# Optimization experiments

Measured on AMD Instinct MI355X. Metric: run time of the kernel, lower is better.

## Reference

```python
import jax, jax.numpy as jnp
import numpy as np

N = 20000   # nodes
E = 320000  # edges
T = 12      # sequence_length
H = 64      # hidden_dim
CIN = 16    # input_dim_per_step
L = 3       # num_st_layers
BN_EPS = 1e-5


def setup_inputs() -> dict:
    key = jax.random.key(0)
    ks = jax.random.split(key, 30)
    s = 0.05
    rn = lambda k, shp: jax.random.normal(k, shp, jnp.float32) * s
    inp = {
        "x": jax.random.normal(ks[0], (N, T * CIN), jnp.float32),
        "edge_index": jax.random.randint(ks[1], (2, E), 0, N, jnp.int32),
        # embedding
        "We": rn(ks[2], (CIN, H)), "be": rn(ks[3], (H,)),
        # stacked per-layer params for the 3 ST layers
        "gcn_W": rn(ks[4], (L, H, H)), "gcn_b": rn(ks[5], (L, H)),
        "conv_w": rn(ks[6], (L, H, H, 3)), "conv_b": rn(ks[7], (L, H)),
        "bn_g": jnp.ones((L, H), jnp.float32), "bn_b": rn(ks[8], (L, H)),
        "bn_m": rn(ks[9], (L, H)),
        "bn_v": jax.random.uniform(ks[10], (L, H), jnp.float32, 0.5, 1.5),
        # temporal attention MLP (H -> H//2 -> 1)
        "ta_w1": rn(ks[11], (H, H // 2)), "ta_b1": rn(ks[12], (H // 2,)),
        "ta_w2": rn(ks[13], (H // 2, 1)), "ta_b2": rn(ks[14], (1,)),
        # feature attention MLP (T -> T//2 -> 1)
        "fa_w1": rn(ks[15], (T, T // 2)), "fa_b1": rn(ks[16], (T // 2,)),
        "fa_w2": rn(ks[17], (T // 2, 1)), "fa_b2": rn(ks[18], (1,)),
        # output MLP (H -> H//2 -> 1)
        "ow1": rn(ks[19], (H, H // 2)), "ob1": rn(ks[20], (H // 2,)),
        "ow2": rn(ks[21], (H // 2, 1)), "ob2": rn(ks[22], (1,)),
    }
    return inp


def reference(x, edge_index, We, be, gcn_W, gcn_b, conv_w, conv_b,
              bn_g, bn_b, bn_m, bn_v, ta_w1, ta_b1, ta_w2, ta_b2,
              fa_w1, fa_b1, fa_w2, fa_b2, ow1, ob1, ow2, ob2):
    n = x.shape[0]
    # --- GCN normalization with self-loops (PyG gcn_norm) ---
    loops = jnp.arange(n, dtype=edge_index.dtype)
    src = jnp.concatenate([edge_index[0], loops])
    dst = jnp.concatenate([edge_index[1], loops])
    deg = jax.ops.segment_sum(jnp.ones_like(src, jnp.float32), dst, num_segments=n)
    dinv = 1.0 / jnp.sqrt(deg)  # deg >= 1 thanks to self-loops
    coef = dinv[src] * dinv[dst]  # [E+N]

    # --- per-timestep embedding (vectorized over t) ---
    xr = x.reshape(n, T, CIN)
    emb = jax.nn.relu(jnp.einsum('ntc,ch->nth', xr, We) + be)  # [N,T,H]
    x_st = emb.reshape(n, T * H)

    # --- ST layers (replicating original row-major .view layout mixing) ---
    for i in range(L):
        xi = x_st.reshape(n, H, T)  # [N,C,T]
        # GCNConv per timestep, batched over t: linear then normalized aggregate
        h = jnp.einsum('nct,cd->ndt', xi, gcn_W[i])          # [N,H,T]
        msg = coef[:, None, None] * h[src]                   # [E+N,H,T]
        agg = jax.ops.segment_sum(msg, dst, num_segments=n) + gcn_b[i][None, :, None]
        # temporal conv (kernel 3, pad 1) over T
        tmp = jax.lax.conv_general_dilated(
            agg, conv_w[i], (1,), [(1, 1)],
            dimension_numbers=('NCH', 'OIH', 'NCH')) + conv_b[i][None, :, None]
        # BatchNorm1d (eval mode: running stats)
        normed = (tmp - bn_m[i][None, :, None]) / jnp.sqrt(bn_v[i][None, :, None] + BN_EPS)
        normed = normed * bn_g[i][None, :, None] + bn_b[i][None, :, None]
        # residual is Identity (in_channels == out_channels)
        x_st = jax.nn.relu(normed + xi).reshape(n, H * T)

    # --- dual attention pooling ---
    xa = x_st.reshape(n, T, H)
    tw = (jnp.einsum('ntm,mk->ntk', jax.nn.relu(jnp.einsum('nth,hm->ntm', xa, ta_w1) + ta_b1), ta_w2) + ta_b2)[..., 0]
    tw = jax.nn.softmax(tw, axis=1)                          # [N,T]
    xt = (xa * tw[..., None]).transpose(0, 2, 1)             # [N,H,T]
    fw = (jnp.einsum('nhm,mk->nhk', jax.nn.relu(jnp.einsum('nht,tm->nhm', xt, fa_w1) + fa_b1), fa_w2) + fa_b2)[..., 0]
    fw = jax.nn.softmax(fw, axis=1)                          # [N,H]
    x_final = jnp.sum(xt * fw[..., None], axis=2)            # [N,H]

    # --- output MLP (dropout is identity in eval) ---
    out = jax.nn.relu(x_final @ ow1 + ob1) @ ow2 + ob2       # [N,1]
    return out
```

## Files before the change

### kernel.cpp

```cpp
#include <hip/hip_runtime.h>
#include <cstddef>
#include <cstdint>

#define T_ 12
#define H_ 64
#define CIN_ 16
#define F_ 768
#define BN_EPS 1e-5f
#define ECAP 80
#define RPITCH 88
#define SLOTS 64

typedef float v2f __attribute__((ext_vector_type(2)));
typedef short s8v __attribute__((ext_vector_type(8)));
typedef float f4v __attribute__((ext_vector_type(4)));

__device__ __forceinline__ unsigned short f2bf(float f) {
    unsigned u = __float_as_uint(f);
    unsigned r = (u + 0x7FFFu + ((u >> 16) & 1u)) >> 16;
    return (unsigned short)r;
}
__device__ __forceinline__ float bf2f(unsigned short h) {
    return __uint_as_float(((unsigned)h) << 16);
}
__device__ __forceinline__ v2f bf2x2(unsigned u) {
    v2f r;
    r.x = __uint_as_float(u << 16);
    r.y = __uint_as_float(u & 0xFFFF0000u);
    return r;
}
__device__ __forceinline__ v2f pkfma(v2f a, v2f b, v2f c) {
    return __builtin_elementwise_fma(a, b, c);
}


__global__ void k_init(int* __restrict__ cursor, int n) {
    int i = blockIdx.x * 256 + threadIdx.x;
    if (i < n) cursor[i] = 0;
}


__global__ __launch_bounds__(256) void k_fused(
        const float* __restrict__ gcn_W, const float* __restrict__ gcn_b,
        const float* __restrict__ conv_w,
        unsigned short* __restrict__ wkA, float* __restrict__ bkp,
        const int* __restrict__ srcv, const int* __restrict__ dstv,
        int* __restrict__ cursor, int* __restrict__ csr_src, int e,
        const float* __restrict__ x, const float* __restrict__ We,
        const float* __restrict__ be, unsigned short* __restrict__ xbf, int nT,
        int nbE) {
    __shared__ float smem[5312];
    int b = blockIdx.x;
    int tid = threadIdx.x;

    if (b < 36) {
        int l = b / 12, k = (b / 4) % 3, cq = b & 3;
        const float* Wg = gcn_W + (size_t)l * 4096;
        const float* cw = conv_w + (size_t)l * 12288;
        float* scwT = smem;
        float* sWg  = smem + 4224;
        float* sgb  = smem + 5248;
        for (int i = tid; i < 4096; i += 256)
            scwT[(i & 63) * 66 + (i >> 6)] = cw[(size_t)i * 3 + k];
        for (int i = tid; i < 1024; i += 256)
            sWg[i] = Wg[cq * 16 * 64 + i];
        if (tid < 64) sgb[tid] = gcn_b[(size_t)l * 64 + tid];
        __syncthreads();
#pragma unroll
        for (int j = 0; j < 4; j++) {
            int idx = j * 256 + tid;
            int cc = idx >> 6;
            int o  = idx & 63;
            float acc = 0.f;
            for (int d = 0; d < 64; d++)
                acc += sWg[cc * 64 + d] * scwT[d * 66 + o];
            int cful = cq * 16 + cc;
            int kidx = k * 64 + cful;
            int ks = kidx >> 5, r = kidx & 31;
            int ln = (r >> 3) * 16 + (o & 15);
            int jj = r & 7;
            wkA[((((size_t)l * 24) + (o >> 4) * 6 + ks) * 64 + ln) * 8 + jj] =
                f2bf(acc);
        }
        if (cq == 0 && tid < 64) {
            int o = tid;
            float acc = 0.f;
            for (int d = 0; d < 64; d++)
                acc += sgb[d] * scwT[d * 66 + o];
            bkp[((size_t)l * 3 + k) * 64 + o] = acc;
        }
        return;
    }
    if (b < 36 + nbE) {
        int i = (b - 36) * 256 + tid;
        if (i < e) {
            int d = dstv[i], s = srcv[i];
            int pos = atomicAdd(&cursor[d], 1);
            if (pos < SLOTS) csr_src[d * SLOTS + pos] = s;
        }
        return;
    }
    float* sW = smem;
    float* sb = smem + 1024;
    for (int i = tid; i < CIN_ * H_; i += 256) sW[i] = We[i];
    if (tid < H_) sb[tid] = be[tid];
    __syncthreads();
    int h4  = tid & 15;
    int ntl = tid >> 4;
    int nt  = (b - 36 - nbE) * 16 + ntl;
    if (nt >= nT) return;
    const float4* xp = (const float4*)(x + (size_t)nt * CIN_);
    float4 xv4[4];
    xv4[0] = xp[0]; xv4[1] = xp[1]; xv4[2] = xp[2]; xv4[3] = xp[3];
    const float* xs = (const float*)xv4;
    float acc[4];
#pragma unroll
    for (int j = 0; j < 4; j++) acc[j] = sb[h4 * 4 + j];
#pragma unroll
    for (int c = 0; c < CIN_; c++) {
        float4 w = *(const float4*)&sW[c * H_ + h4 * 4];
        float xc = xs[c];
        acc[0] += xc * w.x; acc[1] += xc * w.y;
        acc[2] += xc * w.z; acc[3] += xc * w.w;
    }
    ushort4 h;
    h.x = f2bf(fmaxf(acc[0], 0.f)); h.y = f2bf(fmaxf(acc[1], 0.f));
    h.z = f2bf(fmaxf(acc[2], 0.f)); h.w = f2bf(fmaxf(acc[3], 0.f));
    *(ushort4*)&xbf[(size_t)nt * H_ + h4 * 4] = h;
}


__global__ __launch_bounds__(256) void k_post(
        const int* __restrict__ cursor, const int* __restrict__ csr_src,
        float* __restrict__ csr_coef, float* __restrict__ dinv, int n) {
    int i = blockIdx.x * 256 + threadIdx.x;
    int node = i >> 6, slot = i & 63;
    if (node >= n) return;
    int deg = cursor[node];
    float dn = rsqrtf((float)(deg + 1));
    if (slot == 0) dinv[node] = dn;
    if (slot < min(deg, SLOTS)) {
        int s = csr_src[node * SLOTS + slot];
        csr_coef[node * SLOTS + slot] = rsqrtf((float)(cursor[s] + 1)) * dn;
    }
}


#define BPK(aL, aH, c2, u) { \
    aL = pkfma(bf2x2((u).x), c2, aL); \
    aH = pkfma(bf2x2((u).y), c2, aH); }

#define LAYER_GATHER_CONV()                                                    \
    int tid = threadIdx.x;                                                     \
    int n0 = blockIdx.x * 8;                                                   \
    int wave = tid >> 6, lane = tid & 63;                                      \
    int wbase = wave * (ECAP * 2);                                             \
    for (int i = tid; i < 8 * 2 * RPITCH; i += 256) {                          \
        int s = i / (2 * RPITCH);                                              \
        int r = i - s * (2 * RPITCH);                                          \
        int row = (r < RPITCH) ? 0 : 13;                                       \
        int c = (r < RPITCH) ? r : r - RPITCH;                                 \
        sxb[s * 14 * RPITCH + row * RPITCH + c] = 0;                           \
    }                                                                          \
    int begs[2], cnts[2], stgs[2], epos[2];                                    \
    {                                                                          \
        int pos = 0;                                                           \
        for (int si = 0; si < 2; si++) {                                       \
            int nn = n0 + wave * 2 + si; if (nn >= n) nn = n - 1;              \
            int beg = nn * SLOTS;                                              \
            int cnt = min(degv[nn], SLOTS);                                    \
            int stg = min(cnt, ECAP - pos);                                    \
            for (int i = lane; i < stg; i += 64) {                             \
                se[wbase + (pos + i) * 2]     = csr_src[beg + i] * F_;         \
                se[wbase + (pos + i) * 2 + 1] = __float_as_int(csr_coef[beg + i]); \
            }                                                                  \
            begs[si] = beg; cnts[si] = cnt; stgs[si] = stg; epos[si] = pos;    \
            pos += stg;                                                        \
        }                                                                      \
    }                                                                          \
    {                                                                          \
        int i0 = 3 * lane;                                                     \
        for (int si = 0; si < 2; si++) {                                       \
            int s = wave * 2 + si;                                             \
            int nn = n0 + s; if (nn >= n) nn = n - 1;                          \
            float dn = dinv[nn];                                               \
            float cs = dn * dn;                                                \
            v2f cs2 = {cs, cs};                                                \
            const uint2* xp = (const uint2*)(xin + (size_t)nn * F_);           \
            uint2 u0 = xp[i0], u1 = xp[i0 + 1], u2 = xp[i0 + 2];               \
            v2f a0 = bf2x2(u0.x) * cs2, a1 = bf2x2(u0.y) * cs2;                \
            v2f a2 = bf2x2(u1.x) * cs2, a3 = bf2x2(u1.y) * cs2;                \
            v2f a4 = bf2x2(u2.x) * cs2, a5 = bf2x2(u2.y) * cs2;                \
            int cnt = stgs[si];                                                \
            int base = wbase + epos[si] * 2;                                   \
            int e = 0;                                                         \
            for (; e + 3 < cnt; e += 4) {                                      \
                int2 p0 = *(const int2*)&se[base + e * 2];                     \
                int2 p1 = *(const int2*)&se[base + e * 2 + 2];                 \
                int2 p2 = *(const int2*)&se[base + e * 2 + 4];                 \
                int2 p3 = *(const int2*)&se[base + e * 2 + 6];                 \
                const uint2* pA = (const uint2*)(xin + p0.x);                  \
                const uint2* pB = (const uint2*)(xin + p1.x);                  \
                const uint2* pC = (const uint2*)(xin + p2.x);                  \
                const uint2* pD = (const uint2*)(xin + p3.x);                  \
                uint2 uA0 = pA[i0], uA1 = pA[i0 + 1], uA2 = pA[i0 + 2];        \
                uint2 uB0 = pB[i0], uB1 = pB[i0 + 1], uB2 = pB[i0 + 2];        \
                uint2 uC0 = pC[i0], uC1 = pC[i0 + 1], uC2 = pC[i0 + 2];        \
                uint2 uD0 = pD[i0], uD1 = pD[i0 + 1], uD2 = pD[i0 + 2];        \
                float cA = __int_as_float(p0.y), cB = __int_as_float(p1.y);    \
                float cC = __int_as_float(p2.y), cD = __int_as_float(p3.y);    \
                v2f cA2 = {cA, cA}, cB2 = {cB, cB};                            \
                v2f cC2 = {cC, cC}, cD2 = {cD, cD};                            \
                BPK(a0, a1, cA2, uA0) BPK(a2, a3, cA2, uA1) BPK(a4, a5, cA2, uA2) \
                BPK(a0, a1, cB2, uB0) BPK(a2, a3, cB2, uB1) BPK(a4, a5, cB2, uB2) \
                BPK(a0, a1, cC2, uC0) BPK(a2, a3, cC2, uC1) BPK(a4, a5, cC2, uC2) \
                BPK(a0, a1, cD2, uD0) BPK(a2, a3, cD2, uD1) BPK(a4, a5, cD2, uD2) \
            }                                                                  \
            for (; e < cnt; e++) {                                             \
                int2 p0 = *(const int2*)&se[base + e * 2];                     \
                const uint2* pA = (const uint2*)(xin + p0.x);                  \
                uint2 uA0 = pA[i0], uA1 = pA[i0 + 1], uA2 = pA[i0 + 2];        \
                float cA = __int_as_float(p0.y);                               \
                v2f cA2 = {cA, cA};                                            \
                BPK(a0, a1, cA2, uA0) BPK(a2, a3, cA2, uA1) BPK(a4, a5, cA2, uA2) \
            }                                                                  \
            for (int g = begs[si] + stgs[si]; g < begs[si] + cnts[si]; g++) {  \
                int srcO = csr_src[g] * F_;                                    \
                float cf = csr_coef[g];                                        \
                const uint2* pA = (const uint2*)(xin + srcO);                  \
                uint2 uA0 = pA[i0], uA1 = pA[i0 + 1], uA2 = pA[i0 + 2];        \
                v2f cf2 = {cf, cf};                                            \
                BPK(a0, a1, cf2, uA0) BPK(a2, a3, cf2, uA1) BPK(a4, a5, cf2, uA2) \
            }                                                                  \
            unsigned short* wp = &sxb[s * 14 * RPITCH + RPITCH + lane];        \
            float vals[12] = {a0.x, a0.y, a1.x, a1.y, a2.x, a2.y,              \
                              a3.x, a3.y, a4.x, a4.y, a5.x, a5.y};             \
            for (int t = 0; t < 12; t++) wp[t * RPITCH] = f2bf(vals[t]);       \
        }                                                                      \
    }                                                                          \
    __syncthreads();                                                           \
    int mt = wave;                                                             \
    int q = lane >> 4;                                                         \
    int l15 = lane & 15;                                                       \
    s8v afr[6];                                                                \
    const s8v* Ap = (const s8v*)wkA;                                           \
    for (int ks = 0; ks < 6; ks++) afr[ks] = Ap[(mt * 6 + ks) * 64 + lane];    \
    int obase = mt * 16 + q * 4;                                               \
    float scl[4], shf[4], ball[4], bk0a[4], bk2a[4];                           \
    for (int r = 0; r < 4; r++) {                                              \
        int o = obase + r;                                                     \
        float sc = bng[o] * rsqrtf(bnv[o] + BN_EPS);                           \
        scl[r] = sc;                                                           \
        shf[r] = bnb[o] - bnm[o] * sc;                                         \
        float b0 = bkp[o], b1 = bkp[64 + o], b2 = bkp[128 + o];                \
        ball[r] = cb[o] + b0 + b1 + b2;                                        \
        bk0a[r] = b0; bk2a[r] = b2;                                            \
    }                                                                          \
    f4v accv[6];                                                               \
    for (int nt = 0; nt < 6; nt++) {                                           \
        int nidx = nt * 16 + l15;                                              \
        int s = nidx / 12, t = nidx - 12 * s;                                  \
        const s8v* bp = (const s8v*)&sxb[s * 14 * RPITCH + t * RPITCH + q * 8];\
        f4v acc = {0.f, 0.f, 0.f, 0.f};                                        \
        acc = __builtin_amdgcn_mfma_f32_16x16x32_bf16(afr[0], bp[0],  acc, 0, 0, 0); \
        acc = __builtin_amdgcn_mfma_f32_16x16x32_bf16(afr[1], bp[4],  acc, 0, 0, 0); \
        acc = __builtin_amdgcn_mfma_f32_16x16x32_bf16(afr[2], bp[11], acc, 0, 0, 0); \
        acc = __builtin_amdgcn_mfma_f32_16x16x32_bf16(afr[3], bp[15], acc, 0, 0, 0); \
        acc = __builtin_amdgcn_mfma_f32_16x16x32_bf16(afr[4], bp[22], acc, 0, 0, 0); \
        acc = __builtin_amdgcn_mfma_f32_16x16x32_bf16(afr[5], bp[26], acc, 0, 0, 0); \
        accv[nt] = acc;                                                        \
    }                                                                          \
    __syncthreads();                                                           \
    for (int nt = 0; nt < 6; nt++) {                                           \
        int nidx = nt * 16 + l15;                                              \
        int s = nidx / 12, t = nidx - 12 * s;                                  \
        unsigned short* dp = &sxb[s * F_ + t];                                 \
        for (int r = 0; r < 4; r++) {                                          \
            float bias = ball[r];                                              \
            if (t == 0)  bias -= bk0a[r];                                      \
            if (t == 11) bias -= bk2a[r];                                      \
            float v = (accv[nt][r] + bias) * scl[r] + shf[r];                  \
            dp[(obase + r) * 12] = f2bf(v);                                    \
        }                                                                      \
    }                                                                          \
    __syncthreads();


__global__ __launch_bounds__(256, 7) void k_layer(
        const unsigned short* __restrict__ xin,
        unsigned short* __restrict__ xout,
        const int* __restrict__ degv, const int* __restrict__ csr_src,
        const float* __restrict__ csr_coef, const float* __restrict__ dinv,
        const unsigned short* __restrict__ wkA,
        const float* __restrict__ bkp, const float* __restrict__ cb,
        const float* __restrict__ bng, const float* __restrict__ bnb,
        const float* __restrict__ bnm, const float* __restrict__ bnv,
        int n) {
    __shared__ __align__(16) unsigned short sxb[8 * 14 * RPITCH];
    __shared__ int se[4 * ECAP * 2];
    LAYER_GATHER_CONV()

#pragma unroll
    for (int cidx = 0; cidx < 3; cidx++) {
        int c = cidx * 256 + tid;
        int s = c / 96, off = c - s * 96;
        int nn = n0 + s;
        if (nn >= n) continue;
        uint4 dv = *(const uint4*)&sxb[s * F_ + off * 8];
        uint4 rv = ((const uint4*)(xin + (size_t)nn * F_))[off];
        uint4 ov;
        unsigned* dvp = (unsigned*)&dv;
        unsigned* rvp = (unsigned*)&rv;
        unsigned* ovp = (unsigned*)&ov;
#pragma unroll
        for (int w = 0; w < 4; w++) {
            v2f d2 = bf2x2(dvp[w]);
            v2f r2 = bf2x2(rvp[w]);
            float lo = fmaxf(d2.x + r2.x, 0.f);
            float hi = fmaxf(d2.y + r2.y, 0.f);
            ovp[w] = (unsigned)f2bf(lo) | ((unsigned)f2bf(hi) << 16);
        }
        *(uint4*)(xout + (size_t)nn * F_ + off * 8) = ov;
    }
}


__global__ __launch_bounds__(256, 6) void k_layer_attn(
        const unsigned short* __restrict__ xin,
        const int* __restrict__ degv, const int* __restrict__ csr_src,
        const float* __restrict__ csr_coef, const float* __restrict__ dinv,
        const unsigned short* __restrict__ wkA,
        const float* __restrict__ bkp, const float* __restrict__ cb,
        const float* __restrict__ bng, const float* __restrict__ bnb,
        const float* __restrict__ bnm, const float* __restrict__ bnv,
        const float* __restrict__ taw1, const float* __restrict__ tab1,
        const float* __restrict__ taw2, const float* __restrict__ tab2,
        const float* __restrict__ faw1, const float* __restrict__ fab1,
        const float* __restrict__ faw2, const float* __restrict__ fab2,
        const float* __restrict__ ow1, const float* __restrict__ ob1,
        const float* __restrict__ ow2, const float* __restrict__ ob2,
        float* __restrict__ out, int n) {
    __shared__ __align__(16) unsigned short sxb[8 * 14 * RPITCH];
    __shared__ int se[4 * ECAP * 2];
    LAYER_GATHER_CONV()

#pragma unroll
    for (int cidx = 0; cidx < 3; cidx++) {
        int c = cidx * 256 + tid;
        int s = c / 96, off = c - s * 96;
        int nn = n0 + s; if (nn >= n) nn = n - 1;
        uint4 dv = *(const uint4*)&sxb[s * F_ + off * 8];
        uint4 rv = ((const uint4*)(xin + (size_t)nn * F_))[off];
        unsigned* dvp = (unsigned*)&dv;
        unsigned* rvp = (unsigned*)&rv;
#pragma unroll
        for (int w = 0; w < 4; w++) {
            v2f d2 = bf2x2(dvp[w]);
            v2f r2 = bf2x2(rvp[w]);
            float lo = fmaxf(d2.x + r2.x, 0.f);
            float hi = fmaxf(d2.y + r2.y, 0.f);
            dvp[w] = (unsigned)f2bf(lo) | ((unsigned)f2bf(hi) << 16);
        }
        *(uint4*)&sxb[s * F_ + off * 8] = dv;
    }
    __syncthreads();

    float* s_tw = (float*)se;
    float* s_xf = (float*)se + 96;

    {
        int s2 = tid >> 5, m = tid & 31;
        float bm = tab1[m];
        v2f aa0 = {bm, bm}, aa1 = aa0, aa2 = aa0;
        v2f aa3 = aa0, aa4 = aa0, aa5 = aa0;
        const unsigned short* xr = &sxb[s2 * F_];
        float tb2 = tab2[0];
        for (int hh = 0; hh < 64; hh++) {
            const uint2* xp2 = (const uint2*)&xr[hh * 12];
            uint2 w0 = xp2[0], w1 = xp2[1], w2 = xp2[2];
            float wv = taw1[hh * 32 + m];
            v2f wv2 = {wv, wv};
            aa0 = pkfma(bf2x2(w0.x), wv2, aa0);
            aa1 = pkfma(bf2x2(w0.y), wv2, aa1);
            aa2 = pkfma(bf2x2(w1.x), wv2, aa2);
            aa3 = pkfma(bf2x2(w1.y), wv2, aa3);
            aa4 = pkfma(bf2x2(w2.x), wv2, aa4);
            aa5 = pkfma(bf2x2(w2.y), wv2, aa5);
        }
        float w2v = taw2[m];
        float av[12] = {aa0.x, aa0.y, aa1.x, aa1.y, aa2.x, aa2.y,
                        aa3.x, aa3.y, aa4.x, aa4.y, aa5.x, aa5.y};
#pragma unroll
        for (int t = 0; t < 12; t++) {
            float p = fmaxf(av[t], 0.f) * w2v;
            p += __shfl_xor(p, 1); p += __shfl_xor(p, 2);
            p += __shfl_xor(p, 4); p += __shfl_xor(p, 8);
            p += __shfl_xor(p, 16);
            if (m == 0) s_tw[s2 * 12 + t] = p + tb2;
        }
    }
    __syncthreads();

    {
        float fb2 = fab2[0];
        for (int qi = 0; qi < 2; qi++) {
            int ss = wave * 2 + qi;
            float tw[12];
#pragma unroll
            for (int t = 0; t < 12; t++) tw[t] = s_tw[ss * 12 + t];
            float mx = tw[0];
#pragma unroll
            for (int t = 1; t < 12; t++) mx = fmaxf(mx, tw[t]);
            float sum = 0.f;
#pragma unroll
            for (int t = 0; t < 12; t++) { tw[t] = __expf(tw[t] - mx); sum += tw[t]; }
            float inv = 1.f / sum;
            const uint2* xp2 = (const uint2*)&sxb[ss * F_ + lane * 12];
            uint2 w0 = xp2[0], w1 = xp2[1], w2 = xp2[2];
            v2f x0 = bf2x2(w0.x), x1 = bf2x2(w0.y), x2 = bf2x2(w1.x);
            v2f x3 = bf2x2(w1.y), x4 = bf2x2(w2.x), x5 = bf2x2(w2.y);
            float xv[12] = {x0.x, x0.y, x1.x, x1.y, x2.x, x2.y,
                            x3.x, x3.y, x4.x, x4.y, x5.x, x5.y};
            float xt[12];
#pragma unroll
            for (int t = 0; t < 12; t++) xt[t] = xv[t] * tw[t] * inv;
            float lf = fb2;
#pragma unroll
            for (int mm = 0; mm < 6; mm++) {
                float v = fab1[mm];
#pragma unroll
                for (int t = 0; t < 12; t++) v += xt[t] * faw1[t * 6 + mm];
                lf += fmaxf(v, 0.f) * faw2[mm];
            }
            float m2v = lf;
#pragma unroll
            for (int off = 32; off >= 1; off >>= 1)
                m2v = fmaxf(m2v, __shfl_xor(m2v, off));
            float ev = __expf(lf - m2v);
            float sev = ev;
#pragma unroll
            for (int off = 32; off >= 1; off >>= 1) sev += __shfl_xor(sev, off);
            float fwv = ev / sev;
            float xs = 0.f;
#pragma unroll
            for (int t = 0; t < 12; t++) xs += xt[t];
            s_xf[ss * 65 + lane] = fwv * xs;
        }
    }
    __syncthreads();

    {
        int s2 = tid >> 5, m = tid & 31;
        float v = ob1[m];
        const float* xfp = &s_xf[s2 * 65];
        for (int hh = 0; hh < 64; hh++) v += xfp[hh] * ow1[hh * 32 + m];
        float p = fmaxf(v, 0.f) * ow2[m];
        p += __shfl_xor(p, 1); p += __shfl_xor(p, 2);
        p += __shfl_xor(p, 4); p += __shfl_xor(p, 8);
        p += __shfl_xor(p, 16);
        if (m == 0 && n0 + s2 < n) out[n0 + s2] = p + ob2[0];
    }
}


extern "C" void kernel_launch(void* const* d_in, const int* in_sizes, int n_in,
                              void* d_out, int out_size, void* d_ws, size_t ws_size,
                              hipStream_t stream) {
    const float* x      = (const float*)d_in[0];
    const int*   ei     = (const int*)d_in[1];
    const float* We     = (const float*)d_in[2];
    const float* be     = (const float*)d_in[3];
    const float* gcn_W  = (const float*)d_in[4];
    const float* gcn_b  = (const float*)d_in[5];
    const float* conv_w = (const float*)d_in[6];
    const float* conv_b = (const float*)d_in[7];
    const float* bn_g   = (const float*)d_in[8];
    const float* bn_b   = (const float*)d_in[9];
    const float* bn_m   = (const float*)d_in[10];
    const float* bn_v   = (const float*)d_in[11];
    const float* ta_w1  = (const float*)d_in[12];
    const float* ta_b1  = (const float*)d_in[13];
    const float* ta_w2  = (const float*)d_in[14];
    const float* ta_b2  = (const float*)d_in[15];
    const float* fa_w1  = (const float*)d_in[16];
    const float* fa_b1  = (const float*)d_in[17];
    const float* fa_w2  = (const float*)d_in[18];
    const float* fa_b2  = (const float*)d_in[19];
    const float* ow1    = (const float*)d_in[20];
    const float* ob1    = (const float*)d_in[21];
    const float* ow2    = (const float*)d_in[22];
    const float* ob2    = (const float*)d_in[23];

    int n = in_sizes[0] / (T_ * CIN_);
    int e = in_sizes[1] / 2;
    const int* srcv = ei;
    const int* dstv = ei + e;

    char* p = (char*)d_ws;
    auto take = [&](size_t bytes) -> void* {
        void* r = (void*)p;
        p += (bytes + 255) & ~(size_t)255;
        return r;
    };
    int*   cursor    = (int*)take((size_t)n * 4);
    float* dinv      = (float*)take((size_t)n * 4);
    int*   csr_src   = (int*)take((size_t)n * SLOTS * 4);
    float* csr_coef  = (float*)take((size_t)n * SLOTS * 4);
    float* bkp       = (float*)take((size_t)3 * 3 * 64 * 4);
    unsigned short* wkA = (unsigned short*)take((size_t)3 * 24 * 64 * 8 * 2);
    unsigned short* xabf = (unsigned short*)take((size_t)n * F_ * 2);
    unsigned short* xbbf = (unsigned short*)take((size_t)n * F_ * 2);

    int nb_n = (n + 255) / 256;
    int nb_e = (e + 255) / 256;
    int nb8  = (n + 7) / 8;
    int nT   = n * T_;
    int nbM  = (nT + 15) / 16;

    k_init<<<nb_n, 256, 0, stream>>>(cursor, n);
    k_fused<<<36 + nb_e + nbM, 256, 0, stream>>>(
        gcn_W, gcn_b, conv_w, wkA, bkp,
        srcv, dstv, cursor, csr_src, e,
        x, We, be, xabf, nT, nb_e);
    k_post<<<(n * SLOTS + 255) / 256, 256, 0, stream>>>(
        cursor, csr_src, csr_coef, dinv, n);

    k_layer<<<nb8, 256, 0, stream>>>(xabf, xbbf, cursor, csr_src, csr_coef,
                                     dinv, wkA, bkp, conv_b,
                                     bn_g, bn_b, bn_m, bn_v, n);
    k_layer<<<nb8, 256, 0, stream>>>(xbbf, xabf, cursor, csr_src, csr_coef,
                                     dinv, wkA + (size_t)1 * 24 * 64 * 8,
                                     bkp + (size_t)1 * 3 * 64,
                                     conv_b + (size_t)1 * H_,
                                     bn_g + (size_t)1 * H_, bn_b + (size_t)1 * H_,
                                     bn_m + (size_t)1 * H_, bn_v + (size_t)1 * H_,
                                     n);
    k_layer_attn<<<nb8, 256, 0, stream>>>(xabf, cursor, csr_src, csr_coef,
                                          dinv, wkA + (size_t)2 * 24 * 64 * 8,
                                          bkp + (size_t)2 * 3 * 64,
                                          conv_b + (size_t)2 * H_,
                                          bn_g + (size_t)2 * H_, bn_b + (size_t)2 * H_,
                                          bn_m + (size_t)2 * H_, bn_v + (size_t)2 * H_,
                                          ta_w1, ta_b1, ta_w2, ta_b2,
                                          fa_w1, fa_b1, fa_w2, fa_b2,
                                          ow1, ob1, ow2, ob2, (float*)d_out, n);
}
```

Before: 403.0 us.

## Split fused gather+conv layer into separate gather and conv kernels

Each ST layer's GCN neighbor aggregation now runs in its own kernel, k_gather. It spreads each node's 768-feature row across 8 blocks with one wave per node, and reads packed (src offset, coef) pairs that k_post precomputes. The aggregated bf16 result goes to a new global buffer, which the conv kernel reads instead of gathering inline. This is meant to raise parallelism and occupancy for the latency-bound gather and to lighten the conv kernels. The cost is an extra round trip of an N×768 bf16 buffer per layer and three more kernel launches.

New measurement: 495.0 us. 1.23x slower.

```diff
diff --git a/kernel.cpp b/kernel.cpp
--- a/kernel.cpp
+++ b/kernel.cpp
@@ -7,7 +7,6 @@
 #define CIN_ 16
 #define F_ 768
 #define BN_EPS 1e-5f
-#define ECAP 80
 #define RPITCH 88
 #define SLOTS 64
 
@@ -132,7 +131,7 @@
 
 __global__ __launch_bounds__(256) void k_post(
         const int* __restrict__ cursor, const int* __restrict__ csr_src,
-        float* __restrict__ csr_coef, float* __restrict__ dinv, int n) {
+        int2* __restrict__ pack, float* __restrict__ dinv, int n) {
     int i = blockIdx.x * 256 + threadIdx.x;
     int node = i >> 6, slot = i & 63;
     if (node >= n) return;
@@ -141,20 +140,66 @@
     if (slot == 0) dinv[node] = dn;
     if (slot < min(deg, SLOTS)) {
         int s = csr_src[node * SLOTS + slot];
-        csr_coef[node * SLOTS + slot] = rsqrtf((float)(cursor[s] + 1)) * dn;
-    }
-}
-
-
-#define BPK(aL, aH, c2, u) { \
-    aL = pkfma(bf2x2((u).x), c2, aL); \
-    aH = pkfma(bf2x2((u).y), c2, aH); }
-
-#define LAYER_GATHER_CONV()                                                    \
+        float cf = rsqrtf((float)(cursor[s] + 1)) * dn;
+        pack[node * SLOTS + slot] = make_int2(s * 384, __float_as_int(cf));
+    }
+}
+
+
+__global__ __launch_bounds__(256, 8) void k_gather(
+        const unsigned short* __restrict__ xin,
+        unsigned short* __restrict__ agg,
+        const int* __restrict__ degv, const int2* __restrict__ pack,
+        const float* __restrict__ dinv, int n) {
+    __shared__ int2 sed[4 * SLOTS];
+    int b = blockIdx.x;
+    int sl = b & 7;
+    int g = b >> 3;
+    int wave = threadIdx.x >> 6, lane = threadIdx.x & 63;
+    int node = g * 4 + wave;
+    if (node >= n) return;
+    int cnt = min(degv[node], SLOTS);
+    if (lane < cnt) sed[wave * SLOTS + lane] = pack[node * SLOTS + lane];
+    int lb = sl * 48 + (lane < 48 ? lane : 47);
+    const unsigned* xu = (const unsigned*)xin;
+    float dn = dinv[node];
+    float cs = dn * dn;
+    v2f cs2 = {cs, cs};
+    v2f acc = bf2x2(xu[node * 384 + lb]) * cs2;
+    const int2* sp = &sed[wave * SLOTS];
+    int e = 0;
+    for (; e + 3 < cnt; e += 4) {
+        int2 p0 = sp[e], p1 = sp[e + 1], p2 = sp[e + 2], p3 = sp[e + 3];
+        unsigned u0 = xu[p0.x + lb];
+        unsigned u1 = xu[p1.x + lb];
+        unsigned u2 = xu[p2.x + lb];
+        unsigned u3 = xu[p3.x + lb];
+        v2f c0 = {__int_as_float(p0.y), __int_as_float(p0.y)};
+        v2f c1 = {__int_as_float(p1.y), __int_as_float(p1.y)};
+        v2f c2 = {__int_as_float(p2.y), __int_as_float(p2.y)};
+        v2f c3 = {__int_as_float(p3.y), __int_as_float(p3.y)};
+        acc = pkfma(bf2x2(u0), c0, acc);
+        acc = pkfma(bf2x2(u1), c1, acc);
+        acc = pkfma(bf2x2(u2), c2, acc);
+        acc = pkfma(bf2x2(u3), c3, acc);
+    }
+    for (; e < cnt; e++) {
+        int2 p0 = sp[e];
+        unsigned u0 = xu[p0.x + lb];
+        v2f c0 = {__int_as_float(p0.y), __int_as_float(p0.y)};
+        acc = pkfma(bf2x2(u0), c0, acc);
+    }
+    if (lane < 48) {
+        unsigned o = (unsigned)f2bf(acc.x) | ((unsigned)f2bf(acc.y) << 16);
+        ((unsigned*)agg)[node * 384 + lb] = o;
+    }
+}
+
+
+#define CONV_CORE()                                                            \
     int tid = threadIdx.x;                                                     \
     int n0 = blockIdx.x * 8;                                                   \
     int wave = tid >> 6, lane = tid & 63;                                      \
-    int wbase = wave * (ECAP * 2);                                             \
     for (int i = tid; i < 8 * 2 * RPITCH; i += 256) {                          \
         int s = i / (2 * RPITCH);                                              \
         int r = i - s * (2 * RPITCH);                                          \
@@ -162,80 +207,26 @@
         int c = (r < RPITCH) ? r : r - RPITCH;                                 \
         sxb[s * 14 * RPITCH + row * RPITCH + c] = 0;                           \
     }                                                                          \
-    int begs[2], cnts[2], stgs[2], epos[2];                                    \
-    {                                                                          \
-        int pos = 0;                                                           \
-        for (int si = 0; si < 2; si++) {                                       \
-            int nn = n0 + wave * 2 + si; if (nn >= n) nn = n - 1;              \
-            int beg = nn * SLOTS;                                              \
-            int cnt = min(degv[nn], SLOTS);                                    \
-            int stg = min(cnt, ECAP - pos);                                    \
-            for (int i = lane; i < stg; i += 64) {                             \
-                se[wbase + (pos + i) * 2]     = csr_src[beg + i] * F_;         \
-                se[wbase + (pos + i) * 2 + 1] = __float_as_int(csr_coef[beg + i]); \
-            }                                                                  \
-            begs[si] = beg; cnts[si] = cnt; stgs[si] = stg; epos[si] = pos;    \
-            pos += stg;                                                        \
-        }                                                                      \
-    }                                                                          \
     {                                                                          \
         int i0 = 3 * lane;                                                     \
         for (int si = 0; si < 2; si++) {                                       \
             int s = wave * 2 + si;                                             \
             int nn = n0 + s; if (nn >= n) nn = n - 1;                          \
-            float dn = dinv[nn];                                               \
-            float cs = dn * dn;                                                \
-            v2f cs2 = {cs, cs};                                                \
-            const uint2* xp = (const uint2*)(xin + (size_t)nn * F_);           \
-            uint2 u0 = xp[i0], u1 = xp[i0 + 1], u2 = xp[i0 + 2];               \
-            v2f a0 = bf2x2(u0.x) * cs2, a1 = bf2x2(u0.y) * cs2;                \
-            v2f a2 = bf2x2(u1.x) * cs2, a3 = bf2x2(u1.y) * cs2;                \
-            v2f a4 = bf2x2(u2.x) * cs2, a5 = bf2x2(u2.y) * cs2;                \
-            int cnt = stgs[si];                                                \
-            int base = wbase + epos[si] * 2;                                   \
-            int e = 0;                                                         \
-            for (; e + 3 < cnt; e += 4) {                                      \
-                int2 p0 = *(const int2*)&se[base + e * 2];                     \
-                int2 p1 = *(const int2*)&se[base + e * 2 + 2];                 \
-                int2 p2 = *(const int2*)&se[base + e * 2 + 4];                 \
-                int2 p3 = *(const int2*)&se[base + e * 2 + 6];                 \
-                const uint2* pA = (const uint2*)(xin + p0.x);                  \
-                const uint2* pB = (const uint2*)(xin + p1.x);                  \
-                const uint2* pC = (const uint2*)(xin + p2.x);                  \
-                const uint2* pD = (const uint2*)(xin + p3.x);                  \
-                uint2 uA0 = pA[i0], uA1 = pA[i0 + 1], uA2 = pA[i0 + 2];        \
-                uint2 uB0 = pB[i0], uB1 = pB[i0 + 1], uB2 = pB[i0 + 2];        \
-                uint2 uC0 = pC[i0], uC1 = pC[i0 + 1], uC2 = pC[i0 + 2];        \
-                uint2 uD0 = pD[i0], uD1 = pD[i0 + 1], uD2 = pD[i0 + 2];        \
-                float cA = __int_as_float(p0.y), cB = __int_as_float(p1.y);    \
-                float cC = __int_as_float(p2.y), cD = __int_as_float(p3.y);    \
-                v2f cA2 = {cA, cA}, cB2 = {cB, cB};                            \
-                v2f cC2 = {cC, cC}, cD2 = {cD, cD};                            \
-                BPK(a0, a1, cA2, uA0) BPK(a2, a3, cA2, uA1) BPK(a4, a5, cA2, uA2) \
-                BPK(a0, a1, cB2, uB0) BPK(a2, a3, cB2, uB1) BPK(a4, a5, cB2, uB2) \
-                BPK(a0, a1, cC2, uC0) BPK(a2, a3, cC2, uC1) BPK(a4, a5, cC2, uC2) \
-                BPK(a0, a1, cD2, uD0) BPK(a2, a3, cD2, uD1) BPK(a4, a5, cD2, uD2) \
-            }                                                                  \
-            for (; e < cnt; e++) {                                             \
-                int2 p0 = *(const int2*)&se[base + e * 2];                     \
-                const uint2* pA = (const uint2*)(xin + p0.x);                  \
-                uint2 uA0 = pA[i0], uA1 = pA[i0 + 1], uA2 = pA[i0 + 2];        \
-                float cA = __int_as_float(p0.y);                               \
-                v2f cA2 = {cA, cA};                                            \
-                BPK(a0, a1, cA2, uA0) BPK(a2, a3, cA2, uA1) BPK(a4, a5, cA2, uA2) \
-            }                                                                  \
-            for (int g = begs[si] + stgs[si]; g < begs[si] + cnts[si]; g++) {  \
-                int srcO = csr_src[g] * F_;                                    \
-                float cf = csr_coef[g];                                        \
-                const uint2* pA = (const uint2*)(xin + srcO);                  \
-                uint2 uA0 = pA[i0], uA1 = pA[i0 + 1], uA2 = pA[i0 + 2];        \
-                v2f cf2 = {cf, cf};                                            \
-                BPK(a0, a1, cf2, uA0) BPK(a2, a3, cf2, uA1) BPK(a4, a5, cf2, uA2) \
-            }                                                                  \
+            const uint2* ap = (const uint2*)(agg + (size_t)nn * F_);           \
+            uint2 u0 = ap[i0], u1 = ap[i0 + 1], u2 = ap[i0 + 2];               \
             unsigned short* wp = &sxb[s * 14 * RPITCH + RPITCH + lane];        \
-            float vals[12] = {a0.x, a0.y, a1.x, a1.y, a2.x, a2.y,              \
-                              a3.x, a3.y, a4.x, a4.y, a5.x, a5.y};             \
-            for (int t = 0; t < 12; t++) wp[t * RPITCH] = f2bf(vals[t]);       \
+            wp[0]           = (unsigned short)u0.x;                            \
+            wp[RPITCH]      = (unsigned short)(u0.x >> 16);                    \
+            wp[2 * RPITCH]  = (unsigned short)u0.y;                            \
+            wp[3 * RPITCH]  = (unsigned short)(u0.y >> 16);                    \
+            wp[4 * RPITCH]  = (unsigned short)u1.x;                            \
+            wp[5 * RPITCH]  = (unsigned short)(u1.x >> 16);                    \
+            wp[6 * RPITCH]  = (unsigned short)u1.y;                            \
+            wp[7 * RPITCH]  = (unsigned short)(u1.y >> 16);                    \
+            wp[8 * RPITCH]  = (unsigned short)u2.x;                            \
+            wp[9 * RPITCH]  = (unsigned short)(u2.x >> 16);                    \
+            wp[10 * RPITCH] = (unsigned short)u2.y;                            \
+            wp[11 * RPITCH] = (unsigned short)(u2.y >> 16);                    \
         }                                                                      \
     }                                                                          \
     __syncthreads();                                                           \
@@ -286,19 +277,17 @@
     __syncthreads();
 
 
-__global__ __launch_bounds__(256, 7) void k_layer(
+__global__ __launch_bounds__(256, 8) void k_conv(
+        const unsigned short* __restrict__ agg,
         const unsigned short* __restrict__ xin,
         unsigned short* __restrict__ xout,
-        const int* __restrict__ degv, const int* __restrict__ csr_src,
-        const float* __restrict__ csr_coef, const float* __restrict__ dinv,
         const unsigned short* __restrict__ wkA,
         const float* __restrict__ bkp, const float* __restrict__ cb,
         const float* __restrict__ bng, const float* __restrict__ bnb,
         const float* __restrict__ bnm, const float* __restrict__ bnv,
         int n) {
     __shared__ __align__(16) unsigned short sxb[8 * 14 * RPITCH];
-    __shared__ int se[4 * ECAP * 2];
-    LAYER_GATHER_CONV()
+    CONV_CORE()
 
 #pragma unroll
     for (int cidx = 0; cidx < 3; cidx++) {
@@ -325,10 +314,9 @@
 }
 
 
-__global__ __launch_bounds__(256, 6) void k_layer_attn(
+__global__ __launch_bounds__(256, 7) void k_conv_attn(
+        const unsigned short* __restrict__ agg,
         const unsigned short* __restrict__ xin,
-        const int* __restrict__ degv, const int* __restrict__ csr_src,
-        const float* __restrict__ csr_coef, const float* __restrict__ dinv,
         const unsigned short* __restrict__ wkA,
         const float* __restrict__ bkp, const float* __restrict__ cb,
         const float* __restrict__ bng, const float* __restrict__ bnb,
@@ -341,8 +329,8 @@
         const float* __restrict__ ow2, const float* __restrict__ ob2,
         float* __restrict__ out, int n) {
     __shared__ __align__(16) unsigned short sxb[8 * 14 * RPITCH];
-    __shared__ int se[4 * ECAP * 2];
-    LAYER_GATHER_CONV()
+    __shared__ float sft[96 + 520];
+    CONV_CORE()
 
 #pragma unroll
     for (int cidx = 0; cidx < 3; cidx++) {
@@ -365,8 +353,8 @@
     }
     __syncthreads();
 
-    float* s_tw = (float*)se;
-    float* s_xf = (float*)se + 96;
+    float* s_tw = sft;
+    float* s_xf = sft + 96;
 
     {
         int s2 = tid >> 5, m = tid & 31;
@@ -505,15 +493,17 @@
     int*   cursor    = (int*)take((size_t)n * 4);
     float* dinv      = (float*)take((size_t)n * 4);
     int*   csr_src   = (int*)take((size_t)n * SLOTS * 4);
-    float* csr_coef  = (float*)take((size_t)n * SLOTS * 4);
+    int2*  pack      = (int2*)take((size_t)n * SLOTS * 8);
     float* bkp       = (float*)take((size_t)3 * 3 * 64 * 4);
-    unsigned short* wkA = (unsigned short*)take((size_t)3 * 24 * 64 * 8 * 2);
+    unsigned short* wkA  = (unsigned short*)take((size_t)3 * 24 * 64 * 8 * 2);
     unsigned short* xabf = (unsigned short*)take((size_t)n * F_ * 2);
     unsigned short* xbbf = (unsigned short*)take((size_t)n * F_ * 2);
+    unsigned short* aggb = (unsigned short*)take((size_t)n * F_ * 2);
 
     int nb_n = (n + 255) / 256;
     int nb_e = (e + 255) / 256;
     int nb8  = (n + 7) / 8;
+    int nbG  = 8 * ((n + 3) / 4);
     int nT   = n * T_;
     int nbM  = (nT + 15) / 16;
 
@@ -523,25 +513,27 @@
         srcv, dstv, cursor, csr_src, e,
         x, We, be, xabf, nT, nb_e);
     k_post<<<(n * SLOTS + 255) / 256, 256, 0, stream>>>(
-        cursor, csr_src, csr_coef, dinv, n);
-
-    k_layer<<<nb8, 256, 0, stream>>>(xabf, xbbf, cursor, csr_src, csr_coef,
-                                     dinv, wkA, bkp, conv_b,
-                                     bn_g, bn_b, bn_m, bn_v, n);
-    k_layer<<<nb8, 256, 0, stream>>>(xbbf, xabf, cursor, csr_src, csr_coef,
-                                     dinv, wkA + (size_t)1 * 24 * 64 * 8,
-                                     bkp + (size_t)1 * 3 * 64,
-                                     conv_b + (size_t)1 * H_,
-                                     bn_g + (size_t)1 * H_, bn_b + (size_t)1 * H_,
-                                     bn_m + (size_t)1 * H_, bn_v + (size_t)1 * H_,
-                                     n);
-    k_layer_attn<<<nb8, 256, 0, stream>>>(xabf, cursor, csr_src, csr_coef,
-                                          dinv, wkA + (size_t)2 * 24 * 64 * 8,
-                                          bkp + (size_t)2 * 3 * 64,
-                                          conv_b + (size_t)2 * H_,
-                                          bn_g + (size_t)2 * H_, bn_b + (size_t)2 * H_,
-                                          bn_m + (size_t)2 * H_, bn_v + (size_t)2 * H_,
-                                          ta_w1, ta_b1, ta_w2, ta_b2,
-                                          fa_w1, fa_b1, fa_w2, fa_b2,
-                                          ow1, ob1, ow2, ob2, (float*)d_out, n);
-}
+        cursor, csr_src, pack, dinv, n);
+
+    k_gather<<<nbG, 256, 0, stream>>>(xabf, aggb, cursor, pack, dinv, n);
+    k_conv<<<nb8, 256, 0, stream>>>(aggb, xabf, xbbf, wkA, bkp, conv_b,
+                                    bn_g, bn_b, bn_m, bn_v, n);
+    k_gather<<<nbG, 256, 0, stream>>>(xbbf, aggb, cursor, pack, dinv, n);
+    k_conv<<<nb8, 256, 0, stream>>>(aggb, xbbf, xabf,
+                                    wkA + (size_t)1 * 24 * 64 * 8,
+                                    bkp + (size_t)1 * 3 * 64,
+                                    conv_b + (size_t)1 * H_,
+                                    bn_g + (size_t)1 * H_, bn_b + (size_t)1 * H_,
+                                    bn_m + (size_t)1 * H_, bn_v + (size_t)1 * H_,
+                                    n);
+    k_gather<<<nbG, 256, 0, stream>>>(xabf, aggb, cursor, pack, dinv, n);
+    k_conv_attn<<<nb8, 256, 0, stream>>>(aggb, xabf,
+                                         wkA + (size_t)2 * 24 * 64 * 8,
+                                         bkp + (size_t)2 * 3 * 64,
+                                         conv_b + (size_t)2 * H_,
+                                         bn_g + (size_t)2 * H_, bn_b + (size_t)2 * H_,
+                                         bn_m + (size_t)2 * H_, bn_v + (size_t)2 * H_,
+                                         ta_w1, ta_b1, ta_w2, ta_b2,
+                                         fa_w1, fa_b1, fa_w2, fa_b2,
+                                         ow1, ob1, ow2, ob2, (float*)d_out, n);
+}
```
